# Kernel optimization log

Measured on AMD Instinct MI355X. Metric: run time of the kernel, lower is better.

## Reference

```python
import jax, jax.numpy as jnp
import numpy as np

N = 200_000   # total nodes
K = 50_000    # masked (target) nodes; multiple of num_targets
D = 256       # feature dim
M = 1_000     # meta nodes (dynamic param table rows)
T = 2         # num_targets


def setup_inputs() -> dict:
    key = jax.random.key(0)
    ks = jax.random.split(key, 16)
    inp = {}
    names = ['feat00', 'feat01', 'feat10', 'feat11', 'feat20', 'feat21']
    for i, n in enumerate(names):
        inp[n] = jax.random.normal(ks[i], (N, D), dtype=jnp.float32)
    for i, n in enumerate(['w0', 'w1', 'w2']):
        inp[n] = jax.random.normal(ks[6 + i], (M, D), dtype=jnp.float32)
    for i, n in enumerate(['b0', 'b1', 'b2']):
        inp[n] = jax.random.normal(ks[9 + i], (M, 1), dtype=jnp.float32)
    # symbols: first K nodes alternate target symbols 0,1 -> mask hits exactly K nodes
    sym = np.full((N,), 7, dtype=np.int64)
    sym[:K] = np.arange(K) % T
    inp['symbols'] = jnp.asarray(sym)
    inp['meta_node_id'] = jax.random.randint(ks[12], (N,), 0, M, dtype=jnp.int64)
    inp['sym_buf'] = jnp.arange(T, dtype=jnp.int64)  # registered buffer self.symbols
    inp['num_masked'] = K  # static masked count (python int for jit-static shapes)
    return inp


def reference(feat00, feat01, feat10, feat11, feat20, feat21,
              w0, w1, w2, b0, b1, b2,
              symbols, meta_node_id, sym_buf, num_masked):
    feats = [[feat00, feat01], [feat10, feat11], [feat20, feat21]]
    ws = [w0, w1, w2]
    bs = [b0, b1, b2]
    # mask = (symbols.view(-1,1) == self.symbols).any(-1)
    mask = (symbols[:, None] == sym_buf[None, :]).any(-1)
    idx = jnp.nonzero(mask, size=num_masked)[0]          # [K] masked node ids
    masked_id = meta_node_id[idx]                        # [K]
    outputs = []
    for feat, w, b in zip(feats, ws, bs):
        weight = w[masked_id].reshape(num_masked, -1)    # [K, D] gathered dynamic weight
        bias = b[masked_id]                              # [K, 1] gathered dynamic bias
        for layer_feat in feat:
            lf = layer_feat[idx]                         # [K, D]
            outputs.append((lf * weight).sum(-1, keepdims=True) + bias)
    out = jnp.stack(outputs, axis=0).mean(axis=0)        # [K, 1] mean over blocks*layers
    return out.reshape(-1, T)                            # [K/T, num_targets]
```

## Files before the change

kernel.cpp:

```cpp
#include <hip/hip_runtime.h>


typedef float v4f __attribute__((ext_vector_type(4)));

__global__ void count_kernel(const int* __restrict__ symbols,
                             const int* __restrict__ sym_buf,
                             int T, int N, int chunk,
                             int* __restrict__ counts) {
    __shared__ int sbuf[64];
    int Tc = T > 64 ? 64 : T;
    if ((int)threadIdx.x < Tc) sbuf[threadIdx.x] = sym_buf[threadIdx.x];
    __syncthreads();

    int c = blockIdx.x;
    int start = c * chunk;
    int end = min(start + chunk, N);
    int cnt = 0;
    for (int e = start + (int)threadIdx.x; e < end; e += blockDim.x) {
        int s = symbols[e];
        bool hit = false;
        for (int t = 0; t < Tc; ++t) hit = hit || (s == sbuf[t]);
        if (!hit && T > 64)
            for (int t = 64; t < T; ++t) hit = hit || (s == sym_buf[t]);
        cnt += hit ? 1 : 0;
    }
    for (int off = 32; off >= 1; off >>= 1) cnt += __shfl_down(cnt, off);
    __shared__ int lds[4];
    int lane = threadIdx.x & 63, wv = threadIdx.x >> 6;
    if (lane == 0) lds[wv] = cnt;
    __syncthreads();
    if (threadIdx.x == 0) counts[c] = lds[0] + lds[1] + lds[2] + lds[3];
}

__global__ void write_kernel(const int* __restrict__ symbols,
                             const int* __restrict__ sym_buf,
                             int T, int N, int chunk,
                             const int* __restrict__ counts,
                             int* __restrict__ idx, int K) {
    __shared__ int sbuf[64];
    __shared__ int waveTot[4];
    __shared__ int pre[4];
    __shared__ int baseSh;
    int Tc = T > 64 ? 64 : T;
    if ((int)threadIdx.x < Tc) sbuf[threadIdx.x] = sym_buf[threadIdx.x];

    int c = blockIdx.x;
    int lane = threadIdx.x & 63, wv = threadIdx.x >> 6;

    int v = ((int)threadIdx.x < c) ? counts[threadIdx.x] : 0;
    for (int off = 32; off >= 1; off >>= 1) v += __shfl_down(v, off);
    if (lane == 0) pre[wv] = v;
    __syncthreads();
    if (threadIdx.x == 0) baseSh = pre[0] + pre[1] + pre[2] + pre[3];
    __syncthreads();

    int start = c * chunk;
    int end = min(start + chunk, N);
    for (int s = start; s < end; s += blockDim.x) {
        int e = s + (int)threadIdx.x;
        bool hit = false;
        if (e < end) {
            int sym = symbols[e];
            for (int t = 0; t < Tc; ++t) hit = hit || (sym == sbuf[t]);
            if (!hit && T > 64)
                for (int t = 64; t < T; ++t) hit = hit || (sym == sym_buf[t]);
        }
        unsigned long long bal = __ballot(hit);
        int lanePrefix = __popcll(bal & ((1ull << lane) - 1ull));
        int waveCount  = __popcll(bal);
        if (lane == 0) waveTot[wv] = waveCount;
        __syncthreads();
        int wavePrefix = 0;
        for (int w = 0; w < wv; ++w) wavePrefix += waveTot[w];
        int total = waveTot[0] + waveTot[1] + waveTot[2] + waveTot[3];
        if (hit) {
            int pos = baseSh + wavePrefix + lanePrefix;
            if (pos < K) idx[pos] = e;
        }
        __syncthreads();
        if (threadIdx.x == 0) baseSh += total;
        __syncthreads();
    }
}

__global__ __launch_bounds__(256) void dot_kernel(
    const float* __restrict__ f00, const float* __restrict__ f01,
    const float* __restrict__ f10, const float* __restrict__ f11,
    const float* __restrict__ f20, const float* __restrict__ f21,
    const float* __restrict__ w0, const float* __restrict__ w1,
    const float* __restrict__ w2,
    const float* __restrict__ b0, const float* __restrict__ b1,
    const float* __restrict__ b2,
    const int* __restrict__ meta, const int* __restrict__ idx,
    float* __restrict__ out, int K, int D) {
    int wv   = threadIdx.x >> 6;
    int lane = threadIdx.x & 63;
    int k = blockIdx.x * 4 + wv;
    if (k >= K) return;
    int id  = idx[k];
    int mid = meta[id];
    float s = 0.0f;
    for (int d0 = lane * 4; d0 < D; d0 += 256) {
        long long fo = (long long)id  * D + d0;
        long long wo = (long long)mid * D + d0;
        v4f W, A, B;
        W = *(const v4f*)(w0 + wo);
        A = __builtin_nontemporal_load((const v4f*)(f00 + fo));
        B = __builtin_nontemporal_load((const v4f*)(f01 + fo));
        s += (A.x + B.x) * W.x + (A.y + B.y) * W.y
           + (A.z + B.z) * W.z + (A.w + B.w) * W.w;
        W = *(const v4f*)(w1 + wo);
        A = __builtin_nontemporal_load((const v4f*)(f10 + fo));
        B = __builtin_nontemporal_load((const v4f*)(f11 + fo));
        s += (A.x + B.x) * W.x + (A.y + B.y) * W.y
           + (A.z + B.z) * W.z + (A.w + B.w) * W.w;
        W = *(const v4f*)(w2 + wo);
        A = __builtin_nontemporal_load((const v4f*)(f20 + fo));
        B = __builtin_nontemporal_load((const v4f*)(f21 + fo));
        s += (A.x + B.x) * W.x + (A.y + B.y) * W.y
           + (A.z + B.z) * W.z + (A.w + B.w) * W.w;
    }
    for (int off = 32; off >= 1; off >>= 1) s += __shfl_down(s, off);
    if (lane == 0) {
        float bias = b0[mid] + b1[mid] + b2[mid];
        out[k] = s * (1.0f / 6.0f) + bias * (1.0f / 3.0f);
    }
}

extern "C" void kernel_launch(void* const* d_in, const int* in_sizes, int n_in,
                              void* d_out, int out_size, void* d_ws, size_t ws_size,
                              hipStream_t stream) {
    const float* f00 = (const float*)d_in[0];
    const float* f01 = (const float*)d_in[1];
    const float* f10 = (const float*)d_in[2];
    const float* f11 = (const float*)d_in[3];
    const float* f20 = (const float*)d_in[4];
    const float* f21 = (const float*)d_in[5];
    const float* w0  = (const float*)d_in[6];
    const float* w1  = (const float*)d_in[7];
    const float* w2  = (const float*)d_in[8];
    const float* b0  = (const float*)d_in[9];
    const float* b1  = (const float*)d_in[10];
    const float* b2  = (const float*)d_in[11];
    const int* symbols = (const int*)d_in[12];
    const int* meta    = (const int*)d_in[13];
    const int* sym_buf = (const int*)d_in[14];

    const int K = out_size;
    const int D = in_sizes[6] / in_sizes[9];
    const int N = in_sizes[0] / D;
    const int T = in_sizes[14];

    int* idx     = (int*)d_ws;
    int* counts  = idx + K;

    hipMemsetAsync(idx, 0, (size_t)K * sizeof(int), stream);

    const int B = 256;
    const int chunk = (N + B - 1) / B;
    count_kernel<<<B, 256, 0, stream>>>(symbols, sym_buf, T, N, chunk, counts);
    write_kernel<<<B, 256, 0, stream>>>(symbols, sym_buf, T, N, chunk, counts, idx, K);

    int blocks = (K + 3) / 4;
    dot_kernel<<<blocks, 256, 0, stream>>>(f00, f01, f10, f11, f20, f21,
                                           w0, w1, w2, b0, b1, b2,
                                           meta, idx, (float*)d_out, K, D);
}
```

Measured before the change: 757.6 us.

## Process two rows per wave in a grid-stride dot kernel with plain loads

The dot kernel becomes a grid-stride loop capped at 2048 blocks, and each wave handles two masked rows per iteration so more independent loads are in flight. Nontemporal loads are replaced with ordinary cached loads, and the bias loads are issued before the dot loop. The aim is more memory-level parallelism and less per-block launch overhead on this gather-bound kernel. In exchange it uses more registers and drops the cache-bypass hint on the streamed feature reads.

```diff
diff --git a/kernel.cpp b/kernel.cpp
--- a/kernel.cpp
+++ b/kernel.cpp
@@ -95,35 +95,69 @@
     float* __restrict__ out, int K, int D) {
     int wv   = threadIdx.x >> 6;
     int lane = threadIdx.x & 63;
-    int k = blockIdx.x * 4 + wv;
-    if (k >= K) return;
-    int id  = idx[k];
-    int mid = meta[id];
-    float s = 0.0f;
-    for (int d0 = lane * 4; d0 < D; d0 += 256) {
-        long long fo = (long long)id  * D + d0;
-        long long wo = (long long)mid * D + d0;
-        v4f W, A, B;
-        W = *(const v4f*)(w0 + wo);
-        A = __builtin_nontemporal_load((const v4f*)(f00 + fo));
-        B = __builtin_nontemporal_load((const v4f*)(f01 + fo));
-        s += (A.x + B.x) * W.x + (A.y + B.y) * W.y
-           + (A.z + B.z) * W.z + (A.w + B.w) * W.w;
-        W = *(const v4f*)(w1 + wo);
-        A = __builtin_nontemporal_load((const v4f*)(f10 + fo));
-        B = __builtin_nontemporal_load((const v4f*)(f11 + fo));
-        s += (A.x + B.x) * W.x + (A.y + B.y) * W.y
-           + (A.z + B.z) * W.z + (A.w + B.w) * W.w;
-        W = *(const v4f*)(w2 + wo);
-        A = __builtin_nontemporal_load((const v4f*)(f20 + fo));
-        B = __builtin_nontemporal_load((const v4f*)(f21 + fo));
-        s += (A.x + B.x) * W.x + (A.y + B.y) * W.y
-           + (A.z + B.z) * W.z + (A.w + B.w) * W.w;
-    }
-    for (int off = 32; off >= 1; off >>= 1) s += __shfl_down(s, off);
-    if (lane == 0) {
-        float bias = b0[mid] + b1[mid] + b2[mid];
-        out[k] = s * (1.0f / 6.0f) + bias * (1.0f / 3.0f);
+    int gw      = blockIdx.x * 4 + wv;
+    int stride2 = gridDim.x * 4 * 2;
+
+    for (int k0 = gw * 2; k0 < K; k0 += stride2) {
+        int k1 = k0 + 1;
+        bool has1 = (k1 < K);
+        int id0  = idx[k0];
+        int mid0 = meta[id0];
+        int id1  = has1 ? idx[k1] : id0;
+        int mid1 = has1 ? meta[id1] : mid0;
+
+        float bias0 = b0[mid0] + b1[mid0] + b2[mid0];
+        float bias1 = b0[mid1] + b1[mid1] + b2[mid1];
+
+        float s0 = 0.0f, s1 = 0.0f;
+        for (int d = lane * 4; d < D; d += 256) {
+            long long fo0 = (long long)id0  * D + d;
+            long long wo0 = (long long)mid0 * D + d;
+            long long fo1 = (long long)id1  * D + d;
+            long long wo1 = (long long)mid1 * D + d;
+            v4f W, A, B;
+
+            W = *(const v4f*)(w0 + wo0);
+            A = *(const v4f*)(f00 + fo0);
+            B = *(const v4f*)(f01 + fo0);
+            s0 += (A.x + B.x) * W.x + (A.y + B.y) * W.y
+                + (A.z + B.z) * W.z + (A.w + B.w) * W.w;
+            W = *(const v4f*)(w1 + wo0);
+            A = *(const v4f*)(f10 + fo0);
+            B = *(const v4f*)(f11 + fo0);
+            s0 += (A.x + B.x) * W.x + (A.y + B.y) * W.y
+                + (A.z + B.z) * W.z + (A.w + B.w) * W.w;
+            W = *(const v4f*)(w2 + wo0);
+            A = *(const v4f*)(f20 + fo0);
+            B = *(const v4f*)(f21 + fo0);
+            s0 += (A.x + B.x) * W.x + (A.y + B.y) * W.y
+                + (A.z + B.z) * W.z + (A.w + B.w) * W.w;
+
+            W = *(const v4f*)(w0 + wo1);
+            A = *(const v4f*)(f00 + fo1);
+            B = *(const v4f*)(f01 + fo1);
+            s1 += (A.x + B.x) * W.x + (A.y + B.y) * W.y
+                + (A.z + B.z) * W.z + (A.w + B.w) * W.w;
+            W = *(const v4f*)(w1 + wo1);
+            A = *(const v4f*)(f10 + fo1);
+            B = *(const v4f*)(f11 + fo1);
+            s1 += (A.x + B.x) * W.x + (A.y + B.y) * W.y
+                + (A.z + B.z) * W.z + (A.w + B.w) * W.w;
+            W = *(const v4f*)(w2 + wo1);
+            A = *(const v4f*)(f20 + fo1);
+            B = *(const v4f*)(f21 + fo1);
+            s1 += (A.x + B.x) * W.x + (A.y + B.y) * W.y
+                + (A.z + B.z) * W.z + (A.w + B.w) * W.w;
+        }
+
+        for (int off = 32; off >= 1; off >>= 1) {
+            s0 += __shfl_down(s0, off);
+            s1 += __shfl_down(s1, off);
+        }
+        if (lane == 0) {
+            out[k0] = s0 * (1.0f / 6.0f) + bias0 * (1.0f / 3.0f);
+            if (has1) out[k1] = s1 * (1.0f / 6.0f) + bias1 * (1.0f / 3.0f);
+        }
     }
 }
 
@@ -161,7 +195,9 @@
     count_kernel<<<B, 256, 0, stream>>>(symbols, sym_buf, T, N, chunk, counts);
     write_kernel<<<B, 256, 0, stream>>>(symbols, sym_buf, T, N, chunk, counts, idx, K);
 
-    int blocks = (K + 3) / 4;
+    int kpairs  = (K + 1) / 2;
+    int kblocks = (kpairs + 3) / 4;
+    int blocks  = kblocks < 2048 ? kblocks : 2048;
     dot_kernel<<<blocks, 256, 0, stream>>>(f00, f01, f10, f11, f20, f21,
                                            w0, w1, w2, b0, b1, b2,
                                            meta, idx, (float*)d_out, K, D);
```

Result: slower. 779.3 us (+2.9%).
